# Performance work log

Hardware: AMD Instinct MI355X
Metric: run time of the kernel (lower is better)

Reference implementation:

```python
import jax, jax.numpy as jnp
import numpy as np

T, C, H, N = 1024, 2048, 32, 64
D_LORA, D_G = 64, 128

def _ln(x, w, b, eps=1e-5):
    m = x.mean(-1, keepdims=True)
    v = ((x - m) ** 2).mean(-1, keepdims=True)
    return (x - m) * jax.lax.rsqrt(v + eps) * w + b

def setup_inputs():
    key = jax.random.key(0)
    ks = iter(jax.random.split(key, 48))
    rn = lambda shape, s=1.0: jax.random.normal(next(ks), shape, dtype=jnp.float32) * s
    return {
        "x": rn((T, C)),
        "x_prev_att": rn((C,)),
        "vk_state": rn((H, N, N), 0.1),
        "x_prev_ffn": rn((C,)),
        "v_first": rn((T, C)),
        "ln1_w": jnp.ones((C,), jnp.float32), "ln1_b": jnp.zeros((C,), jnp.float32),
        "x_r": rn((C,), 0.1), "x_w": rn((C,), 0.1), "x_k": rn((C,), 0.1),
        "x_v": rn((C,), 0.1), "x_a": rn((C,), 0.1), "x_g": rn((C,), 0.1),
        "w0": rn((C,), 0.1), "w1": rn((C, D_LORA), 0.02), "w2": rn((D_LORA, C), 0.02),
        "a0": rn((C,), 0.1), "a1": rn((C, D_LORA), 0.02), "a2": rn((D_LORA, C), 0.02),
        "v0": rn((C,), 0.1), "v1": rn((C, D_LORA), 0.02), "v2": rn((D_LORA, C), 0.02),
        "g1": rn((C, D_G), 0.02), "g2": rn((D_G, C), 0.02),
        "k_k": rn((C,), 0.1), "k_a": rn((C,), 0.1), "r_k": rn((C,), 0.1),
        "R_": rn((C, C), 0.02), "K_": rn((C, C), 0.02),
        "V_": rn((C, C), 0.02), "O_": rn((C, C), 0.02),
        "lnx_w": jnp.ones((C,), jnp.float32), "lnx_b": jnp.zeros((C,), jnp.float32),
        "ln2_w": jnp.ones((C,), jnp.float32), "ln2_b": jnp.zeros((C,), jnp.float32),
        "ffn_x_k": rn((C,), 0.1),
        "ffn_K": rn((C, 4 * C), 0.02), "ffn_V": rn((4 * C, C), 0.02),
    }

def reference(x, x_prev_att, vk_state, x_prev_ffn, v_first, ln1_w, ln1_b,
              x_r, x_w, x_k, x_v, x_a, x_g, w0, w1, w2, a0, a1, a2,
              v0, v1, v2, g1, g2, k_k, k_a, r_k, R_, K_, V_, O_,
              lnx_w, lnx_b, ln2_w, ln2_b, ffn_x_k, ffn_K, ffn_V):
    # ---- TMix: RWKV-7 time mixing (layer_id = 1, so v_first blend is active) ----
    xln = _ln(x, ln1_w, ln1_b)                                  # [T, C]
    dx = jnp.concatenate([x_prev_att[None, :], xln[:-1]], axis=0) - xln  # token shift
    xr, xw, xk, xv, xa, xg = (xln + dx * m for m in (x_r, x_w, x_k, x_v, x_a, x_g))
    r = xr @ R_
    w = jnp.tanh(xw @ w1) @ w2
    k = xk @ K_
    v = xv @ V_
    a = jax.nn.sigmoid(a0 + (xa @ a1) @ a2)
    g = jax.nn.sigmoid(xg @ g1) @ g2
    kk = (k * k_k).reshape(T, H, N)
    kk = kk / jnp.maximum(jnp.linalg.norm(kk, axis=-1, keepdims=True), 1e-12)  # L2 normalize per head
    k = k * (1.0 + (a - 1.0) * k_a)
    v = v + (v_first - v) * jax.nn.sigmoid(v0 + (xv @ v1) @ v2)  # layer_id != 0 path
    w = jnp.exp(-0.606531 * jax.nn.sigmoid(w0 + w))               # per-channel decay in (0,1)
    rh, kh, vh = r.reshape(T, H, N), k.reshape(T, H, N), v.reshape(T, H, N)
    ah, wh = a.reshape(T, H, N), w.reshape(T, H, N)

    def step(state, inp):
        # state: [H, N, N]; generalized delta rule: state*w + state@(-kk)(kk*a)^T + v k^T
        w_t, kk_t, a_t, k_t, v_t, r_t = inp
        ab = jnp.einsum('hi,hj->hij', -kk_t, kk_t * a_t)
        vk = jnp.einsum('hi,hj->hij', v_t, k_t)
        state = state * w_t[:, None, :] + jnp.einsum('hij,hjk->hik', state, ab) + vk
        return state, jnp.einsum('hij,hj->hi', state, r_t)

    vk_state, outs = jax.lax.scan(step, vk_state, (wh, kk, ah, kh, vh, rh))  # outs: [T, H, N]
    # group norm over H groups, eps = 0.00064, affine per-channel
    m = outs.mean(-1, keepdims=True)
    var = ((outs - m) ** 2).mean(-1, keepdims=True)
    gn = ((outs - m) * jax.lax.rsqrt(var + 0.00064)).reshape(T, C) * lnx_w + lnx_b
    bonus = ((r * k * r_k).reshape(T, H, N).sum(-1, keepdims=True) * vh).reshape(T, C)
    x = x + ((gn + bonus) * g) @ O_
    # ---- CMix: gated squared-ReLU MLP ----
    xln2 = _ln(x, ln2_w, ln2_b)
    dx2 = jnp.concatenate([x_prev_ffn[None, :], xln2[:-1]], axis=0) - xln2
    kf = jax.nn.relu((xln2 + dx2 * ffn_x_k) @ ffn_K) ** 2
    x = x + kf @ ffn_V
    return x
```

## Files before the change

kernel.cpp:

```cpp
#include <hip/hip_runtime.h>
#include <hip/hip_bf16.h>


#define T_ 1024
#define C_ 2048
#define H_ 32
#define NH 64

typedef __attribute__((ext_vector_type(8))) short short8v;
typedef __attribute__((ext_vector_type(4))) float f32x4;

__device__ __forceinline__ float bf2f(unsigned short u) {
  union { float f; unsigned int i; } c; c.i = ((unsigned int)u) << 16; return c.f;
}
__device__ __forceinline__ unsigned short f2bf(float f) {
  union { float f; unsigned int i; } c; c.f = f;
  unsigned int x = c.i;
  return (unsigned short)((x + 0x7fffu + ((x >> 16) & 1u)) >> 16);
}
__device__ __forceinline__ float sigm(float x) { return 1.f / (1.f + __expf(-x)); }

__device__ __forceinline__ void load8bf(const unsigned short* p, float* o) {
  union { int4 v; unsigned short u[8]; } c;
  c.v = *(const int4*)p;
#pragma unroll
  for (int i = 0; i < 8; ++i) o[i] = bf2f(c.u[i]);
}
__device__ __forceinline__ void store8bf(unsigned short* p, const float* o) {
  union { int4 v; unsigned short u[8]; } c;
#pragma unroll
  for (int i = 0; i < 8; ++i) c.u[i] = f2bf(o[i]);
  *(int4*)p = c.v;
}
__device__ __forceinline__ void load8f(const float* p, float* o) {
  float4 a = ((const float4*)p)[0], b = ((const float4*)p)[1];
  o[0] = a.x; o[1] = a.y; o[2] = a.z; o[3] = a.w;
  o[4] = b.x; o[5] = b.y; o[6] = b.z; o[7] = b.w;
}
__device__ __forceinline__ void load4f(const float* p, float* o) {
  float4 a = *(const float4*)p;
  o[0] = a.x; o[1] = a.y; o[2] = a.z; o[3] = a.w;
}

#define GLD16(g, l)                                                        \
  __builtin_amdgcn_global_load_lds(                                        \
      (const __attribute__((address_space(1))) void*)(g),                  \
      (__attribute__((address_space(3))) void*)(l), 16, 0, 0)

__global__ __launch_bounds__(256) void ln_kernel(const float* __restrict__ x,
                                                 const float* __restrict__ w,
                                                 const float* __restrict__ b,
                                                 unsigned short* __restrict__ out) {
  int t = blockIdx.x, tid = threadIdx.x;
  const float* xr = x + (size_t)t * C_;
  float v[8];
  load8f(xr + tid * 8, v);
  float s = 0.f, q = 0.f;
#pragma unroll
  for (int i = 0; i < 8; ++i) { s += v[i]; q += v[i] * v[i]; }
  for (int m = 1; m < 64; m <<= 1) { s += __shfl_xor(s, m); q += __shfl_xor(q, m); }
  __shared__ float rs[4], rq[4];
  if ((tid & 63) == 0) { rs[tid >> 6] = s; rq[tid >> 6] = q; }
  __syncthreads();
  s = rs[0] + rs[1] + rs[2] + rs[3];
  q = rq[0] + rq[1] + rq[2] + rq[3];
  float mean = s * (1.f / C_);
  float var = q * (1.f / C_) - mean * mean;
  float rstd = rsqrtf(var + 1e-5f);
  int c = tid * 8;
  float o[8];
#pragma unroll
  for (int i = 0; i < 8; ++i) o[i] = (v[i] - mean) * rstd * w[c + i] + b[c + i];
  store8bf(out + (size_t)t * C_ + c, o);
}

__global__ __launch_bounds__(256) void mix6_kernel(
    const unsigned short* __restrict__ xln, const float* __restrict__ xprev,
    const float* __restrict__ mr, const float* __restrict__ mw,
    const float* __restrict__ mk, const float* __restrict__ mv,
    const float* __restrict__ ma, const float* __restrict__ mg,
    unsigned short* xr, unsigned short* xw, unsigned short* xk,
    unsigned short* xv, unsigned short* xa, unsigned short* xg) {
  int t = blockIdx.x, tid = threadIdx.x, c = tid * 8;
  float cur[8], prv[8];
  load8bf(xln + (size_t)t * C_ + c, cur);
  if (t == 0) load8f(xprev + c, prv);
  else load8bf(xln + (size_t)(t - 1) * C_ + c, prv);
  float cf[8], o[8];
  const float* coefs[6] = {mr, mw, mk, mv, ma, mg};
  unsigned short* outs6[6] = {xr, xw, xk, xv, xa, xg};
#pragma unroll
  for (int a = 0; a < 6; ++a) {
    load8f(coefs[a] + c, cf);
#pragma unroll
    for (int i = 0; i < 8; ++i) o[i] = cur[i] + (prv[i] - cur[i]) * cf[i];
    store8bf(outs6[a] + (size_t)t * C_ + c, o);
  }
}

__global__ __launch_bounds__(256) void mix1_kernel(
    const unsigned short* __restrict__ xln, const float* __restrict__ xprev,
    const float* __restrict__ coef, unsigned short* __restrict__ o) {
  int t = blockIdx.x, tid = threadIdx.x, c = tid * 8;
  float cur[8], prv[8], cf[8], o8[8];
  load8bf(xln + (size_t)t * C_ + c, cur);
  if (t == 0) load8f(xprev + c, prv);
  else load8bf(xln + (size_t)(t - 1) * C_ + c, prv);
  load8f(coef + c, cf);
#pragma unroll
  for (int i = 0; i < 8; ++i) o8[i] = cur[i] + (prv[i] - cur[i]) * cf[i];
  store8bf(o + (size_t)t * C_ + c, o8);
}

__global__ __launch_bounds__(256) void transpose_kernel(
    const float* in0, const float* in1, const float* in2,
    unsigned short* o0, unsigned short* o1, unsigned short* o2,
    int R, int Cc) {
  const float* in = blockIdx.z == 0 ? in0 : (blockIdx.z == 1 ? in1 : in2);
  unsigned short* out = blockIdx.z == 0 ? o0 : (blockIdx.z == 1 ? o1 : o2);
  __shared__ __align__(16) unsigned short tile[64][80];
  int c0 = blockIdx.x * 64, r0 = blockIdx.y * 64;
  int rr = threadIdx.x >> 4, cq = threadIdx.x & 15;
#pragma unroll
  for (int i = 0; i < 4; ++i) {
    int r = rr + i * 16;
    float4 v = *(const float4*)(in + (size_t)(r0 + r) * Cc + c0 + cq * 4);
    tile[cq * 4 + 0][r] = f2bf(v.x);
    tile[cq * 4 + 1][r] = f2bf(v.y);
    tile[cq * 4 + 2][r] = f2bf(v.z);
    tile[cq * 4 + 3][r] = f2bf(v.w);
  }
  __syncthreads();
  int cr = threadIdx.x >> 2, rg = threadIdx.x & 3;
  int4 w0 = *(const int4*)&tile[cr][rg * 16];
  int4 w1 = *(const int4*)&tile[cr][rg * 16 + 8];
  unsigned short* op = out + (size_t)(c0 + cr) * R + r0 + rg * 16;
  *(int4*)op = w0;
  *(int4*)(op + 8) = w1;
}

template <int EPI>
__global__ __launch_bounds__(256) void gemm2_kernel(
    const unsigned short* A0, const unsigned short* A1, const unsigned short* A2,
    const unsigned short* B0, const unsigned short* B1, const unsigned short* B2,
    void* C0, void* C1, void* C2, const float* __restrict__ addsrc,
    int M, int K, int N) {
  int z = blockIdx.z;
  const unsigned short* A = z == 0 ? A0 : (z == 1 ? A1 : A2);
  const unsigned short* Bt = z == 0 ? B0 : (z == 1 ? B1 : B2);
  void* Cout = z == 0 ? C0 : (z == 1 ? C1 : C2);
  __shared__ __align__(16) unsigned short As[128 * 32];
  __shared__ __align__(16) unsigned short Bs[128 * 32];
  const int tid = threadIdx.x, lane = tid & 63, wid = tid >> 6;
  const int bm = blockIdx.y * 128, bn = blockIdx.x * 128;
  const int wr = wid >> 1, wc = wid & 1;
  const int mrow = lane & 15, krow = lane >> 4;
  f32x4 acc[4][4] = {};
  for (int kt = 0; kt < K; kt += 32) {
#pragma unroll
    for (int q = 0; q < 2; ++q) {
      int s = q * 2048 + tid * 8;
      int m = s >> 5, k = s & 31;
      GLD16(A + (size_t)(bm + m) * K + kt + k, &As[s]);
      GLD16(Bt + (size_t)(bn + m) * K + kt + k, &Bs[s]);
    }
    __syncthreads();
    short8v af[4], bfrag[4];
#pragma unroll
    for (int i = 0; i < 4; ++i)
      af[i] = *(const short8v*)&As[(wr * 64 + i * 16 + mrow) * 32 + krow * 8];
#pragma unroll
    for (int j = 0; j < 4; ++j)
      bfrag[j] = *(const short8v*)&Bs[(wc * 64 + j * 16 + mrow) * 32 + krow * 8];
#pragma unroll
    for (int i = 0; i < 4; ++i)
#pragma unroll
      for (int j = 0; j < 4; ++j)
        acc[i][j] = __builtin_amdgcn_mfma_f32_16x16x32_bf16(af[i], bfrag[j], acc[i][j], 0, 0, 0);
    __syncthreads();
  }
#pragma unroll
  for (int i = 0; i < 4; ++i)
#pragma unroll
    for (int j = 0; j < 4; ++j)
#pragma unroll
      for (int e = 0; e < 4; ++e) {
        int grow = bm + wr * 64 + i * 16 + (lane >> 4) * 4 + e;
        int gcol = bn + wc * 64 + j * 16 + (lane & 15);
        size_t off = (size_t)grow * N + gcol;
        float v = acc[i][j][e];
        if constexpr (EPI == 0) ((float*)Cout)[off] = v;
        else if constexpr (EPI == 1) ((float*)Cout)[off] = addsrc[off] + v;
        else { float r = v > 0.f ? v : 0.f; ((unsigned short*)Cout)[off] = f2bf(r * r); }
      }
}

__global__ __launch_bounds__(256) void gemm2ks_kernel(
    const unsigned short* __restrict__ A, const unsigned short* __restrict__ Bt,
    float* __restrict__ P, int M, int KH, int Ktot, int N) {
  int kz = blockIdx.z;
  const size_t kbase = (size_t)kz * KH;
  __shared__ __align__(16) unsigned short As[128 * 32];
  __shared__ __align__(16) unsigned short Bs[128 * 32];
  const int tid = threadIdx.x, lane = tid & 63, wid = tid >> 6;
  const int bm = blockIdx.y * 128, bn = blockIdx.x * 128;
  const int wr = wid >> 1, wc = wid & 1;
  const int mrow = lane & 15, krow = lane >> 4;
  f32x4 acc[4][4] = {};
  for (int kt = 0; kt < KH; kt += 32) {
#pragma unroll
    for (int q = 0; q < 2; ++q) {
      int s = q * 2048 + tid * 8;
      int m = s >> 5, k = s & 31;
      GLD16(A + (size_t)(bm + m) * Ktot + kbase + kt + k, &As[s]);
      GLD16(Bt + (size_t)(bn + m) * Ktot + kbase + kt + k, &Bs[s]);
    }
    __syncthreads();
    short8v af[4], bfrag[4];
#pragma unroll
    for (int i = 0; i < 4; ++i)
      af[i] = *(const short8v*)&As[(wr * 64 + i * 16 + mrow) * 32 + krow * 8];
#pragma unroll
    for (int j = 0; j < 4; ++j)
      bfrag[j] = *(const short8v*)&Bs[(wc * 64 + j * 16 + mrow) * 32 + krow * 8];
#pragma unroll
    for (int i = 0; i < 4; ++i)
#pragma unroll
      for (int j = 0; j < 4; ++j)
        acc[i][j] = __builtin_amdgcn_mfma_f32_16x16x32_bf16(af[i], bfrag[j], acc[i][j], 0, 0, 0);
    __syncthreads();
  }
  float* Pz = P + (size_t)kz * M * N;
#pragma unroll
  for (int i = 0; i < 4; ++i)
#pragma unroll
    for (int j = 0; j < 4; ++j)
#pragma unroll
      for (int e = 0; e < 4; ++e) {
        int grow = bm + wr * 64 + i * 16 + (lane >> 4) * 4 + e;
        int gcol = bn + wc * 64 + j * 16 + (lane & 15);
        Pz[(size_t)grow * N + gcol] = acc[i][j][e];
      }
}

__global__ __launch_bounds__(256) void gemm2ks3_kernel(
    const unsigned short* A0, const unsigned short* A1, const unsigned short* A2,
    const unsigned short* B0, const unsigned short* B1, const unsigned short* B2,
    float* __restrict__ P, int M, int KH, int Ktot, int N) {
  int z = blockIdx.z;
  int batch = z % 3, kz = z / 3;
  const unsigned short* A = batch == 0 ? A0 : (batch == 1 ? A1 : A2);
  const unsigned short* Bt = batch == 0 ? B0 : (batch == 1 ? B1 : B2);
  const size_t kbase = (size_t)kz * KH;
  __shared__ __align__(16) unsigned short As[128 * 32];
  __shared__ __align__(16) unsigned short Bs[128 * 32];
  const int tid = threadIdx.x, lane = tid & 63, wid = tid >> 6;
  const int bm = blockIdx.y * 128, bn = blockIdx.x * 128;
  const int wr = wid >> 1, wc = wid & 1;
  const int mrow = lane & 15, krow = lane >> 4;
  f32x4 acc[4][4] = {};
  for (int kt = 0; kt < KH; kt += 32) {
#pragma unroll
    for (int q = 0; q < 2; ++q) {
      int s = q * 2048 + tid * 8;
      int m = s >> 5, k = s & 31;
      GLD16(A + (size_t)(bm + m) * Ktot + kbase + kt + k, &As[s]);
      GLD16(Bt + (size_t)(bn + m) * Ktot + kbase + kt + k, &Bs[s]);
    }
    __syncthreads();
    short8v af[4], bfrag[4];
#pragma unroll
    for (int i = 0; i < 4; ++i)
      af[i] = *(const short8v*)&As[(wr * 64 + i * 16 + mrow) * 32 + krow * 8];
#pragma unroll
    for (int j = 0; j < 4; ++j)
      bfrag[j] = *(const short8v*)&Bs[(wc * 64 + j * 16 + mrow) * 32 + krow * 8];
#pragma unroll
    for (int i = 0; i < 4; ++i)
#pragma unroll
      for (int j = 0; j < 4; ++j)
        acc[i][j] = __builtin_amdgcn_mfma_f32_16x16x32_bf16(af[i], bfrag[j], acc[i][j], 0, 0, 0);
    __syncthreads();
  }
  float* Pz = P + (size_t)z * M * N;
#pragma unroll
  for (int i = 0; i < 4; ++i)
#pragma unroll
    for (int j = 0; j < 4; ++j)
#pragma unroll
      for (int e = 0; e < 4; ++e) {
        int grow = bm + wr * 64 + i * 16 + (lane >> 4) * 4 + e;
        int gcol = bn + wc * 64 + j * 16 + (lane & 15);
        Pz[(size_t)grow * N + gcol] = acc[i][j][e];
      }
}

__global__ __launch_bounds__(256) void addsk3_kernel(float* __restrict__ q) {
  size_t i = ((size_t)blockIdx.x * 256 + threadIdx.x) * 4;
  float4 a = *(const float4*)(q + i);
  float4 b = *(const float4*)(q + i + 3ull * T_ * C_);
  float4 r;
  r.x = a.x + b.x; r.y = a.y + b.y; r.z = a.z + b.z; r.w = a.w + b.w;
  *(float4*)(q + i) = r;
}

__global__ __launch_bounds__(256) void add5_kernel(
    const float* __restrict__ a, const float* __restrict__ p,
    float* __restrict__ o) {
  size_t i = ((size_t)blockIdx.x * 256 + threadIdx.x) * 4;
  const size_t TC = (size_t)T_ * C_;
  float4 va = *(const float4*)(a + i);
  float4 v0 = *(const float4*)(p + i);
  float4 v1 = *(const float4*)(p + i + TC);
  float4 v2 = *(const float4*)(p + i + 2 * TC);
  float4 v3 = *(const float4*)(p + i + 3 * TC);
  float4 r;
  r.x = va.x + v0.x + v1.x + v2.x + v3.x;
  r.y = va.y + v0.y + v1.y + v2.y + v3.y;
  r.z = va.z + v0.z + v1.z + v2.z + v3.z;
  r.w = va.w + v0.w + v1.w + v2.w + v3.w;
  *(float4*)(o + i) = r;
}

__global__ __launch_bounds__(256) void gemm_ks3_kernel(
    const unsigned short* A0, const unsigned short* A1, const unsigned short* A2,
    const unsigned short* B0, const unsigned short* B1, const unsigned short* B2,
    float* P0, float* P1, float* P2, int K, int N) {
  int mz = blockIdx.z >> 3, kz = blockIdx.z & 7;
  const unsigned short* A = mz == 0 ? A0 : (mz == 1 ? A1 : A2);
  const unsigned short* Bt = mz == 0 ? B0 : (mz == 1 ? B1 : B2);
  float* partial = mz == 0 ? P0 : (mz == 1 ? P1 : P2);
  __shared__ __align__(16) unsigned short As[128 * 32];
  __shared__ __align__(16) unsigned short Bs[64 * 32];
  const int tid = threadIdx.x, lane = tid & 63, wid = tid >> 6;
  const int bn = blockIdx.x * 64, bm = blockIdx.y * 128;
  const int wr = wid >> 1, wc = wid & 1;
  const int mrow = lane & 15, krow = lane >> 4;
  f32x4 acc[4][2] = {};
  for (int kt = kz * 256; kt < kz * 256 + 256; kt += 32) {
#pragma unroll
    for (int q = 0; q < 2; ++q) {
      int s = q * 2048 + tid * 8;
      int m = s >> 5, k = s & 31;
      GLD16(A + (size_t)(bm + m) * K + kt + k, &As[s]);
    }
    {
      int s = tid * 8;
      int n = s >> 5, k = s & 31;
      GLD16(Bt + (size_t)(bn + n) * K + kt + k, &Bs[s]);
    }
    __syncthreads();
    short8v af[4], bfrag[2];
#pragma unroll
    for (int i = 0; i < 4; ++i)
      af[i] = *(const short8v*)&As[(wr * 64 + i * 16 + mrow) * 32 + krow * 8];
#pragma unroll
    for (int j = 0; j < 2; ++j)
      bfrag[j] = *(const short8v*)&Bs[(wc * 32 + j * 16 + mrow) * 32 + krow * 8];
#pragma unroll
    for (int i = 0; i < 4; ++i)
#pragma unroll
      for (int j = 0; j < 2; ++j)
        acc[i][j] = __builtin_amdgcn_mfma_f32_16x16x32_bf16(af[i], bfrag[j], acc[i][j], 0, 0, 0);
    __syncthreads();
  }
#pragma unroll
  for (int i = 0; i < 4; ++i)
#pragma unroll
    for (int j = 0; j < 2; ++j)
#pragma unroll
      for (int e = 0; e < 4; ++e) {
        int row = bm + wr * 64 + i * 16 + (lane >> 4) * 4 + e;
        int col = bn + wc * 32 + j * 16 + (lane & 15);
        partial[((size_t)kz * 1024 + row) * N + col] = acc[i][j][e];
      }
}

__global__ __launch_bounds__(256) void gemm_ks_kernel(
    const unsigned short* __restrict__ A, const unsigned short* __restrict__ Bt,
    float* __restrict__ partial, int K, int N) {
  __shared__ __align__(16) unsigned short As[128 * 32];
  __shared__ __align__(16) unsigned short Bs[64 * 32];
  const int tid = threadIdx.x, lane = tid & 63, wid = tid >> 6;
  const int bn = blockIdx.x * 64, bm = blockIdx.y * 128, kz = blockIdx.z;
  const int wr = wid >> 1, wc = wid & 1;
  const int mrow = lane & 15, krow = lane >> 4;
  f32x4 acc[4][2] = {};
  for (int kt = kz * 256; kt < kz * 256 + 256; kt += 32) {
#pragma unroll
    for (int q = 0; q < 2; ++q) {
      int s = q * 2048 + tid * 8;
      int m = s >> 5, k = s & 31;
      GLD16(A + (size_t)(bm + m) * K + kt + k, &As[s]);
    }
    {
      int s = tid * 8;
      int n = s >> 5, k = s & 31;
      GLD16(Bt + (size_t)(bn + n) * K + kt + k, &Bs[s]);
    }
    __syncthreads();
    short8v af[4], bfrag[2];
#pragma unroll
    for (int i = 0; i < 4; ++i)
      af[i] = *(const short8v*)&As[(wr * 64 + i * 16 + mrow) * 32 + krow * 8];
#pragma unroll
    for (int j = 0; j < 2; ++j)
      bfrag[j] = *(const short8v*)&Bs[(wc * 32 + j * 16 + mrow) * 32 + krow * 8];
#pragma unroll
    for (int i = 0; i < 4; ++i)
#pragma unroll
      for (int j = 0; j < 2; ++j)
        acc[i][j] = __builtin_amdgcn_mfma_f32_16x16x32_bf16(af[i], bfrag[j], acc[i][j], 0, 0, 0);
    __syncthreads();
  }
#pragma unroll
  for (int i = 0; i < 4; ++i)
#pragma unroll
    for (int j = 0; j < 2; ++j)
#pragma unroll
      for (int e = 0; e < 4; ++e) {
        int row = bm + wr * 64 + i * 16 + (lane >> 4) * 4 + e;
        int col = bn + wc * 32 + j * 16 + (lane & 15);
        partial[((size_t)kz * 1024 + row) * N + col] = acc[i][j][e];
      }
}

__global__ __launch_bounds__(128) void lora_combine_kernel(
    const float* __restrict__ pw, const float* __restrict__ pa,
    const float* __restrict__ pv, const float* __restrict__ pg,
    unsigned short* __restrict__ hw, unsigned short* __restrict__ ha,
    unsigned short* __restrict__ hv, unsigned short* __restrict__ hg) {
  int t = blockIdx.x, which = blockIdx.y, tid = threadIdx.x;
  int Nl = (which == 3) ? 128 : 64;
  if (tid >= Nl) return;
  const float* p = which == 0 ? pw : which == 1 ? pa : which == 2 ? pv : pg;
  float s = 0.f;
#pragma unroll
  for (int kz = 0; kz < 8; ++kz) s += p[((size_t)kz * 1024 + t) * Nl + tid];
  float r = which == 0 ? tanhf(s) : (which == 3 ? sigm(s) : s);
  unsigned short* o = which == 0 ? hw : which == 1 ? ha : which == 2 ? hv : hg;
  o[t * Nl + tid] = f2bf(r);
}

__global__ __launch_bounds__(256) void post_kernel(
    const float* __restrict__ k_, const float* __restrict__ vraw,
    const float* __restrict__ r_, const float* __restrict__ wpre,
    const float* __restrict__ apre, const float* __restrict__ vpre,
    const float* __restrict__ vfirst, const float* __restrict__ w0,
    const float* __restrict__ a0, const float* __restrict__ v0_,
    const float* __restrict__ k_k, const float* __restrict__ k_a,
    float* __restrict__ scanin) {
  int t = blockIdx.x, tid = threadIdx.x;
  int c = tid * 8, h = tid >> 3, j = c & 63;
  size_t o = (size_t)t * C_ + c;
  float kv[8], vv[8], rv[8], wv[8], av[8], vp[8], vf[8];
  load8f(k_ + o, kv); load8f(vraw + o, vv); load8f(r_ + o, rv);
  load8f(wpre + o, wv); load8f(apre + o, av); load8f(vpre + o, vp);
  load8f(vfirst + o, vf);
  float ckk[8], cka[8], cw0[8], ca0[8], cv0[8];
  load8f(k_k + c, ckk); load8f(k_a + c, cka); load8f(w0 + c, cw0);
  load8f(a0 + c, ca0); load8f(v0_ + c, cv0);
  float kk[8]; float ss = 0.f;
#pragma unroll
  for (int i = 0; i < 8; ++i) { kk[i] = kv[i] * ckk[i]; ss += kk[i] * kk[i]; }
  ss += __shfl_xor(ss, 1); ss += __shfl_xor(ss, 2); ss += __shfl_xor(ss, 4);
  float rdn = 1.f / fmaxf(sqrtf(ss), 1e-12f);
  float sw[8], skn[8], scc[8], sk2[8], sv[8];
#pragma unroll
  for (int i = 0; i < 8; ++i) {
    float kkn = kk[i] * rdn;
    float a = sigm(ca0[i] + av[i]);
    skn[i] = kkn;
    scc[i] = -kkn * a;
    sk2[i] = kv[i] * (1.f + (a - 1.f) * cka[i]);
    float sg = sigm(cv0[i] + vp[i]);
    sv[i] = vv[i] + (vf[i] - vv[i]) * sg;
    sw[i] = __expf(-0.606531f * sigm(cw0[i] + wv[i]));
  }
  float* bp = scanin + ((size_t)h * T_ + t) * 384 + j;
  ((float4*)(bp + 0))[0]   = make_float4(sw[0], sw[1], sw[2], sw[3]);
  ((float4*)(bp + 4))[0]   = make_float4(sw[4], sw[5], sw[6], sw[7]);
  ((float4*)(bp + 64))[0]  = make_float4(skn[0], skn[1], skn[2], skn[3]);
  ((float4*)(bp + 68))[0]  = make_float4(skn[4], skn[5], skn[6], skn[7]);
  ((float4*)(bp + 128))[0] = make_float4(scc[0], scc[1], scc[2], scc[3]);
  ((float4*)(bp + 132))[0] = make_float4(scc[4], scc[5], scc[6], scc[7]);
  ((float4*)(bp + 192))[0] = make_float4(sk2[0], sk2[1], sk2[2], sk2[3]);
  ((float4*)(bp + 196))[0] = make_float4(sk2[4], sk2[5], sk2[6], sk2[7]);
  ((float4*)(bp + 256))[0] = make_float4(sv[0], sv[1], sv[2], sv[3]);
  ((float4*)(bp + 260))[0] = make_float4(sv[4], sv[5], sv[6], sv[7]);
  ((float4*)(bp + 320))[0] = make_float4(rv[0], rv[1], rv[2], rv[3]);
  ((float4*)(bp + 324))[0] = make_float4(rv[4], rv[5], rv[6], rv[7]);
}

struct SR { float wv[4], nv[4], cv[4], kv[4], rv[4], vvv; };

template <int CTRL>
__device__ __forceinline__ float dppadd(float x) {
  int y = __builtin_amdgcn_update_dpp(0, __float_as_int(x), CTRL, 0xF, 0xF, true);
  return x + __int_as_float(y);
}
__device__ __forceinline__ float red16(float x) {
  x = dppadd<0xB1>(x);
  x = dppadd<0x4E>(x);
  x = dppadd<0x140>(x);
  x = dppadd<0x141>(x);
  return x;
}

__device__ __forceinline__ void loadstep(const float* S, SR& R, int p4, int row) {
  load4f(S + p4, R.wv);
  load4f(S + 64 + p4, R.nv);
  load4f(S + 128 + p4, R.cv);
  load4f(S + 192 + p4, R.kv);
  load4f(S + 320 + p4, R.rv);
  R.vvv = S[256 + row];
}

__device__ __forceinline__ void stepcomp(const SR& R, float* st, int part,
                                         float* __restrict__ ob, size_t oidx) {
  float p0 = fmaf(st[0], R.nv[0], 0.f);
  float p1 = fmaf(st[1], R.nv[1], 0.f);
  p0 = fmaf(st[2], R.nv[2], p0);
  p1 = fmaf(st[3], R.nv[3], p1);
  float sa = red16(p0 + p1);
  float s0 = 0.f, s1 = 0.f;
#pragma unroll
  for (int i = 0; i < 4; ++i) {
    float t = fmaf(st[i], R.wv[i], fmaf(sa, R.cv[i], R.vvv * R.kv[i]));
    st[i] = t;
    if (i & 1) s1 = fmaf(t, R.rv[i], s1);
    else s0 = fmaf(t, R.rv[i], s0);
  }
  float so = red16(s0 + s1);
  if (part == 0) ob[oidx] = so;
}

__global__ __launch_bounds__(64) void scan5_kernel(
    const float* __restrict__ scanin, const float* __restrict__ vk0,
    float* __restrict__ outs) {
  int bid = blockIdx.x;
  int h = (bid & 7) + 8 * ((bid >> 3) & 3);
  int rg = bid >> 5;
  int tid = threadIdx.x;
  int part = tid & 15, row = rg * 4 + (tid >> 4);
  int p4 = part * 4;
  float st[4];
  load4f(vk0 + ((size_t)h * NH + row) * NH + p4, st);
  const float* src = scanin + (size_t)h * T_ * 384;
  float* ob = outs + h * NH + row;
  SR A, B, C, D;
  loadstep(src + 0 * 384, A, p4, row);
  loadstep(src + 1 * 384, B, p4, row);
  loadstep(src + 2 * 384, C, p4, row);
  int s = 0;
  for (; s < T_ - 4; s += 4) {
    const float* sp = src + (size_t)s * 384;
    loadstep(sp + 3 * 384, D, p4, row);
    stepcomp(A, st, part, ob, (size_t)(s + 0) * C_);
    loadstep(sp + 4 * 384, A, p4, row);
    stepcomp(B, st, part, ob, (size_t)(s + 1) * C_);
    loadstep(sp + 5 * 384, B, p4, row);
    stepcomp(C, st, part, ob, (size_t)(s + 2) * C_);
    loadstep(sp + 6 * 384, C, p4, row);
    stepcomp(D, st, part, ob, (size_t)(s + 3) * C_);
  }
  loadstep(src + (size_t)(T_ - 1) * 384, D, p4, row);
  stepcomp(A, st, part, ob, (size_t)(s + 0) * C_);
  stepcomp(B, st, part, ob, (size_t)(s + 1) * C_);
  stepcomp(C, st, part, ob, (size_t)(s + 2) * C_);
  stepcomp(D, st, part, ob, (size_t)(s + 3) * C_);
}

__global__ __launch_bounds__(256) void gnb_kernel(
    const float* __restrict__ outs, const float* __restrict__ scanin,
    const float* __restrict__ g, const float* __restrict__ rk,
    const float* __restrict__ gw, const float* __restrict__ gb,
    unsigned short* __restrict__ attin) {
  int t = blockIdx.x, tid = threadIdx.x;
  int c = tid * 8, h = tid >> 3, j = c & 63;
  float o[8], gv[8], rkv[8];
  load8f(outs + (size_t)t * C_ + c, o);
  load8f(g + (size_t)t * C_ + c, gv);
  load8f(rk + c, rkv);
  size_t sbase = ((size_t)h * T_ + t) * 384 + j;
  float rv[8], k2[8], vv[8];
  load8f(scanin + sbase + 320, rv);
  load8f(scanin + sbase + 192, k2);
  load8f(scanin + sbase + 256, vv);
  float s = 0.f, q = 0.f, bs = 0.f;
#pragma unroll
  for (int i = 0; i < 8; ++i) {
    s += o[i]; q += o[i] * o[i];
    bs += rv[i] * k2[i] * rkv[i];
  }
  s += __shfl_xor(s, 1); s += __shfl_xor(s, 2); s += __shfl_xor(s, 4);
  q += __shfl_xor(q, 1); q += __shfl_xor(q, 2); q += __shfl_xor(q, 4);
  bs += __shfl_xor(bs, 1); bs += __shfl_xor(bs, 2); bs += __shfl_xor(bs, 4);
  float mean = s * (1.f / NH);
  float var = q * (1.f / NH) - mean * mean;
  float rstd = rsqrtf(var + 0.00064f);
  float res[8];
#pragma unroll
  for (int i = 0; i < 8; ++i) {
    float gn = (o[i] - mean) * rstd * gw[c + i] + gb[c + i];
    res[i] = (gn + bs * vv[i]) * gv[i];
  }
  store8bf(attin + (size_t)t * C_ + c, res);
}

extern "C" void kernel_launch(void* const* d_in, const int* in_sizes, int n_in,
                              void* d_out, int out_size, void* d_ws, size_t ws_size,
                              hipStream_t stream) {
  const float* x       = (const float*)d_in[0];
  const float* xprev_a = (const float*)d_in[1];
  const float* vk0     = (const float*)d_in[2];
  const float* xprev_f = (const float*)d_in[3];
  const float* vfirst  = (const float*)d_in[4];
  const float* ln1w = (const float*)d_in[5];
  const float* ln1b = (const float*)d_in[6];
  const float* m_r = (const float*)d_in[7];
  const float* m_w = (const float*)d_in[8];
  const float* m_k = (const float*)d_in[9];
  const float* m_v = (const float*)d_in[10];
  const float* m_a = (const float*)d_in[11];
  const float* m_g = (const float*)d_in[12];
  const float* w0 = (const float*)d_in[13];
  const float* w1 = (const float*)d_in[14];
  const float* w2 = (const float*)d_in[15];
  const float* a0 = (const float*)d_in[16];
  const float* a1 = (const float*)d_in[17];
  const float* a2 = (const float*)d_in[18];
  const float* v0 = (const float*)d_in[19];
  const float* v1 = (const float*)d_in[20];
  const float* v2 = (const float*)d_in[21];
  const float* g1 = (const float*)d_in[22];
  const float* g2 = (const float*)d_in[23];
  const float* k_k = (const float*)d_in[24];
  const float* k_a = (const float*)d_in[25];
  const float* r_k = (const float*)d_in[26];
  const float* R_ = (const float*)d_in[27];
  const float* K_ = (const float*)d_in[28];
  const float* V_ = (const float*)d_in[29];
  const float* O_ = (const float*)d_in[30];
  const float* lnxw = (const float*)d_in[31];
  const float* lnxb = (const float*)d_in[32];
  const float* ln2w = (const float*)d_in[33];
  const float* ln2b = (const float*)d_in[34];
  const float* fxk = (const float*)d_in[35];
  const float* fK = (const float*)d_in[36];
  const float* fV = (const float*)d_in[37];
  float* out = (float*)d_out;

  char* ws = (char*)d_ws;
  const size_t MB = 1ull << 20;
  unsigned short* xln   = (unsigned short*)(ws + 0 * MB);
  unsigned short* attin = (unsigned short*)(ws + 0 * MB);
  unsigned short* xr    = (unsigned short*)(ws + 4 * MB);
  unsigned short* xln2  = (unsigned short*)(ws + 4 * MB);
  unsigned short* xw    = (unsigned short*)(ws + 8 * MB);
  unsigned short* xkf   = (unsigned short*)(ws + 8 * MB);
  unsigned short* xk    = (unsigned short*)(ws + 12 * MB);
  unsigned short* xv    = (unsigned short*)(ws + 16 * MB);
  unsigned short* xa    = (unsigned short*)(ws + 20 * MB);
  unsigned short* xg    = (unsigned short*)(ws + 24 * MB);
  float* qRKV  = (float*)(ws + 28 * MB);
  float* r_buf = (float*)(ws + 28 * MB);
  float* k_buf = (float*)(ws + 36 * MB);
  float* v_buf = (float*)(ws + 44 * MB);
  unsigned short* fVt = (unsigned short*)(ws + 28 * MB);
  float* wpre  = (float*)(ws + 52 * MB);
  float* outsb = (float*)(ws + 52 * MB);
  float* apre  = (float*)(ws + 60 * MB);
  float* x_att = (float*)(ws + 60 * MB);
  float* vpre  = (float*)(ws + 68 * MB);
  float* g_buf = (float*)(ws + 76 * MB);
  float* scanin = (float*)(ws + 84 * MB);
  unsigned short* Rt  = (unsigned short*)(ws + 84 * MB);
  unsigned short* Kt  = (unsigned short*)(ws + 92 * MB);
  unsigned short* Vt  = (unsigned short*)(ws + 100 * MB);
  unsigned short* Ot  = (unsigned short*)(ws + 84 * MB);
  float* qO = (float*)(ws + 92 * MB);
  unsigned short* hffn = (unsigned short*)(ws + 84 * MB);
  unsigned short* fKt  = (unsigned short*)(ws + 100 * MB);
  float* pF = (float*)(ws + 100 * MB);
  unsigned short* w1t = (unsigned short*)(ws + 0);
  unsigned short* a1t = (unsigned short*)(ws + 262144);
  unsigned short* v1t = (unsigned short*)(ws + 524288);
  unsigned short* g1t = (unsigned short*)(ws + 786432);
  unsigned short* hwb = (unsigned short*)(ws + 1310720);
  unsigned short* hab = (unsigned short*)(ws + 1441792);
  unsigned short* hvb = (unsigned short*)(ws + 1572864);
  unsigned short* hgb = (unsigned short*)(ws + 1703936);
  float* pw = (float*)(ws + 2 * MB);
  float* pa = (float*)(ws + 4 * MB);
  float* pv = (float*)(ws + 6 * MB);
  float* pg = (float*)(ws + 8 * MB);
  unsigned short* w2t = (unsigned short*)(ws + 12 * MB);
  unsigned short* a2t = (unsigned short*)(ws + 12 * MB + 262144);
  unsigned short* v2t = (unsigned short*)(ws + 12 * MB + 524288);
  unsigned short* g2t = (unsigned short*)(ws + 12 * MB + 786432);

  ln_kernel<<<T_, 256, 0, stream>>>(x, ln1w, ln1b, xln);
  mix6_kernel<<<T_, 256, 0, stream>>>(xln, xprev_a, m_r, m_w, m_k, m_v, m_a, m_g,
                                      xr, xw, xk, xv, xa, xg);
  transpose_kernel<<<dim3(32, 32, 3), 256, 0, stream>>>(R_, K_, V_, Rt, Kt, Vt, C_, C_);
  gemm2ks3_kernel<<<dim3(16, 8, 6), 256, 0, stream>>>(xr, xk, xv, Rt, Kt, Vt,
                                                      qRKV, T_, 1024, C_, C_);
  addsk3_kernel<<<6144, 256, 0, stream>>>(qRKV);
  transpose_kernel<<<dim3(1, 32, 3), 256, 0, stream>>>(w1, a1, v1, w1t, a1t, v1t, C_, 64);
  transpose_kernel<<<dim3(2, 32, 1), 256, 0, stream>>>(g1, g1, g1, g1t, g1t, g1t, C_, 128);
  gemm_ks3_kernel<<<dim3(1, 8, 24), 256, 0, stream>>>(xw, xa, xv, w1t, a1t, v1t,
                                                      pw, pa, pv, C_, 64);
  gemm_ks_kernel<<<dim3(2, 8, 8), 256, 0, stream>>>(xg, g1t, pg, C_, 128);
  lora_combine_kernel<<<dim3(T_, 4), 128, 0, stream>>>(pw, pa, pv, pg, hwb, hab, hvb, hgb);
  transpose_kernel<<<dim3(32, 1, 3), 256, 0, stream>>>(w2, a2, v2, w2t, a2t, v2t, 64, C_);
  transpose_kernel<<<dim3(32, 2, 1), 256, 0, stream>>>(g2, g2, g2, g2t, g2t, g2t, 128, C_);
  gemm2_kernel<0><<<dim3(16, 8, 3), 256, 0, stream>>>(hwb, hab, hvb, w2t, a2t, v2t,
                                                      wpre, apre, vpre, nullptr, T_, 64, C_);
  gemm2_kernel<0><<<dim3(16, 8, 1), 256, 0, stream>>>(hgb, hgb, hgb, g2t, g2t, g2t,
                                                      g_buf, g_buf, g_buf, nullptr, T_, 128, C_);
  post_kernel<<<T_, 256, 0, stream>>>(k_buf, v_buf, r_buf, wpre, apre, vpre, vfirst,
                                      w0, a0, v0, k_k, k_a, scanin);
  scan5_kernel<<<512, 64, 0, stream>>>(scanin, vk0, outsb);
  gnb_kernel<<<T_, 256, 0, stream>>>(outsb, scanin, g_buf, r_k, lnxw, lnxb, attin);
  transpose_kernel<<<dim3(32, 32, 1), 256, 0, stream>>>(O_, O_, O_, Ot, Ot, Ot, C_, C_);
  transpose_kernel<<<dim3(32, 128, 1), 256, 0, stream>>>(fV, fV, fV, fVt, fVt, fVt, 4 * C_, C_);
  gemm2ks_kernel<<<dim3(16, 8, 4), 256, 0, stream>>>(attin, Ot, qO, T_, 512, C_, C_);
  add5_kernel<<<2048, 256, 0, stream>>>(x, qO, x_att);
  ln_kernel<<<T_, 256, 0, stream>>>(x_att, ln2w, ln2b, xln2);
  mix1_kernel<<<T_, 256, 0, stream>>>(xln2, xprev_f, fxk, xkf);
  transpose_kernel<<<dim3(128, 32, 1), 256, 0, stream>>>(fK, fK, fK, fKt, fKt, fKt, C_, 4 * C_);
  gemm2_kernel<2><<<dim3(64, 8, 1), 256, 0, stream>>>(xkf, xkf, xkf, fKt, fKt, fKt,
                                                      hffn, hffn, hffn, nullptr, T_, C_, 4 * C_);
  gemm2ks_kernel<<<dim3(16, 8, 4), 256, 0, stream>>>(hffn, fVt, pF, T_, 2048, 4 * C_, C_);
  add5_kernel<<<2048, 256, 0, stream>>>(x_att, pF, out);
}
```

Before: 514.0 us.

## Double-buffer LDS tiles in all MFMA GEMM kernels to overlap loads with compute

Each bf16 MFMA GEMM variant (batched, split-K and 64-wide split-K) now keeps two LDS buffers for the A and B tiles. The loads for the next K-slice are issued at the top of each iteration, before the MFMA work on the current slice, which drops one barrier per iteration. The aim is to hide global-to-LDS latency behind matrix-core work. In exchange, LDS per block doubles, which may lower how many blocks fit on a CU at once.

```diff
diff --git a/kernel.cpp b/kernel.cpp
--- a/kernel.cpp
+++ b/kernel.cpp
@@ -149,35 +149,41 @@
   const unsigned short* A = z == 0 ? A0 : (z == 1 ? A1 : A2);
   const unsigned short* Bt = z == 0 ? B0 : (z == 1 ? B1 : B2);
   void* Cout = z == 0 ? C0 : (z == 1 ? C1 : C2);
-  __shared__ __align__(16) unsigned short As[128 * 32];
-  __shared__ __align__(16) unsigned short Bs[128 * 32];
+  __shared__ __align__(16) unsigned short As[2][128 * 32];
+  __shared__ __align__(16) unsigned short Bs[2][128 * 32];
   const int tid = threadIdx.x, lane = tid & 63, wid = tid >> 6;
   const int bm = blockIdx.y * 128, bn = blockIdx.x * 128;
   const int wr = wid >> 1, wc = wid & 1;
   const int mrow = lane & 15, krow = lane >> 4;
-  f32x4 acc[4][4] = {};
-  for (int kt = 0; kt < K; kt += 32) {
+  auto stage = [&](int buf, int kt) {
 #pragma unroll
     for (int q = 0; q < 2; ++q) {
       int s = q * 2048 + tid * 8;
       int m = s >> 5, k = s & 31;
-      GLD16(A + (size_t)(bm + m) * K + kt + k, &As[s]);
-      GLD16(Bt + (size_t)(bn + m) * K + kt + k, &Bs[s]);
+      GLD16(A + (size_t)(bm + m) * K + kt + k, &As[buf][s]);
+      GLD16(Bt + (size_t)(bn + m) * K + kt + k, &Bs[buf][s]);
     }
-    __syncthreads();
+  };
+  f32x4 acc[4][4] = {};
+  stage(0, 0);
+  __syncthreads();
+  int buf = 0;
+  for (int kt = 0; kt < K; kt += 32) {
+    if (kt + 32 < K) stage(buf ^ 1, kt + 32);
     short8v af[4], bfrag[4];
 #pragma unroll
     for (int i = 0; i < 4; ++i)
-      af[i] = *(const short8v*)&As[(wr * 64 + i * 16 + mrow) * 32 + krow * 8];
+      af[i] = *(const short8v*)&As[buf][(wr * 64 + i * 16 + mrow) * 32 + krow * 8];
 #pragma unroll
     for (int j = 0; j < 4; ++j)
-      bfrag[j] = *(const short8v*)&Bs[(wc * 64 + j * 16 + mrow) * 32 + krow * 8];
+      bfrag[j] = *(const short8v*)&Bs[buf][(wc * 64 + j * 16 + mrow) * 32 + krow * 8];
 #pragma unroll
     for (int i = 0; i < 4; ++i)
 #pragma unroll
       for (int j = 0; j < 4; ++j)
         acc[i][j] = __builtin_amdgcn_mfma_f32_16x16x32_bf16(af[i], bfrag[j], acc[i][j], 0, 0, 0);
     __syncthreads();
+    buf ^= 1;
   }
 #pragma unroll
   for (int i = 0; i < 4; ++i)
@@ -200,35 +206,41 @@
     float* __restrict__ P, int M, int KH, int Ktot, int N) {
   int kz = blockIdx.z;
   const size_t kbase = (size_t)kz * KH;
-  __shared__ __align__(16) unsigned short As[128 * 32];
-  __shared__ __align__(16) unsigned short Bs[128 * 32];
+  __shared__ __align__(16) unsigned short As[2][128 * 32];
+  __shared__ __align__(16) unsigned short Bs[2][128 * 32];
   const int tid = threadIdx.x, lane = tid & 63, wid = tid >> 6;
   const int bm = blockIdx.y * 128, bn = blockIdx.x * 128;
   const int wr = wid >> 1, wc = wid & 1;
   const int mrow = lane & 15, krow = lane >> 4;
-  f32x4 acc[4][4] = {};
-  for (int kt = 0; kt < KH; kt += 32) {
+  auto stage = [&](int buf, int kt) {
 #pragma unroll
     for (int q = 0; q < 2; ++q) {
       int s = q * 2048 + tid * 8;
       int m = s >> 5, k = s & 31;
-      GLD16(A + (size_t)(bm + m) * Ktot + kbase + kt + k, &As[s]);
-      GLD16(Bt + (size_t)(bn + m) * Ktot + kbase + kt + k, &Bs[s]);
+      GLD16(A + (size_t)(bm + m) * Ktot + kbase + kt + k, &As[buf][s]);
+      GLD16(Bt + (size_t)(bn + m) * Ktot + kbase + kt + k, &Bs[buf][s]);
     }
-    __syncthreads();
+  };
+  f32x4 acc[4][4] = {};
+  stage(0, 0);
+  __syncthreads();
+  int buf = 0;
+  for (int kt = 0; kt < KH; kt += 32) {
+    if (kt + 32 < KH) stage(buf ^ 1, kt + 32);
     short8v af[4], bfrag[4];
 #pragma unroll
     for (int i = 0; i < 4; ++i)
-      af[i] = *(const short8v*)&As[(wr * 64 + i * 16 + mrow) * 32 + krow * 8];
+      af[i] = *(const short8v*)&As[buf][(wr * 64 + i * 16 + mrow) * 32 + krow * 8];
 #pragma unroll
     for (int j = 0; j < 4; ++j)
-      bfrag[j] = *(const short8v*)&Bs[(wc * 64 + j * 16 + mrow) * 32 + krow * 8];
+      bfrag[j] = *(const short8v*)&Bs[buf][(wc * 64 + j * 16 + mrow) * 32 + krow * 8];
 #pragma unroll
     for (int i = 0; i < 4; ++i)
 #pragma unroll
       for (int j = 0; j < 4; ++j)
         acc[i][j] = __builtin_amdgcn_mfma_f32_16x16x32_bf16(af[i], bfrag[j], acc[i][j], 0, 0, 0);
     __syncthreads();
+    buf ^= 1;
   }
   float* Pz = P + (size_t)kz * M * N;
 #pragma unroll
@@ -252,35 +264,41 @@
   const unsigned short* A = batch == 0 ? A0 : (batch == 1 ? A1 : A2);
   const unsigned short* Bt = batch == 0 ? B0 : (batch == 1 ? B1 : B2);
   const size_t kbase = (size_t)kz * KH;
-  __shared__ __align__(16) unsigned short As[128 * 32];
-  __shared__ __align__(16) unsigned short Bs[128 * 32];
+  __shared__ __align__(16) unsigned short As[2][128 * 32];
+  __shared__ __align__(16) unsigned short Bs[2][128 * 32];
   const int tid = threadIdx.x, lane = tid & 63, wid = tid >> 6;
   const int bm = blockIdx.y * 128, bn = blockIdx.x * 128;
   const int wr = wid >> 1, wc = wid & 1;
   const int mrow = lane & 15, krow = lane >> 4;
-  f32x4 acc[4][4] = {};
-  for (int kt = 0; kt < KH; kt += 32) {
+  auto stage = [&](int buf, int kt) {
 #pragma unroll
     for (int q = 0; q < 2; ++q) {
       int s = q * 2048 + tid * 8;
       int m = s >> 5, k = s & 31;
-      GLD16(A + (size_t)(bm + m) * Ktot + kbase + kt + k, &As[s]);
-      GLD16(Bt + (size_t)(bn + m) * Ktot + kbase + kt + k, &Bs[s]);
+      GLD16(A + (size_t)(bm + m) * Ktot + kbase + kt + k, &As[buf][s]);
+      GLD16(Bt + (size_t)(bn + m) * Ktot + kbase + kt + k, &Bs[buf][s]);
     }
-    __syncthreads();
+  };
+  f32x4 acc[4][4] = {};
+  stage(0, 0);
+  __syncthreads();
+  int buf = 0;
+  for (int kt = 0; kt < KH; kt += 32) {
+    if (kt + 32 < KH) stage(buf ^ 1, kt + 32);
     short8v af[4], bfrag[4];
 #pragma unroll
     for (int i = 0; i < 4; ++i)
-      af[i] = *(const short8v*)&As[(wr * 64 + i * 16 + mrow) * 32 + krow * 8];
+      af[i] = *(const short8v*)&As[buf][(wr * 64 + i * 16 + mrow) * 32 + krow * 8];
 #pragma unroll
     for (int j = 0; j < 4; ++j)
-      bfrag[j] = *(const short8v*)&Bs[(wc * 64 + j * 16 + mrow) * 32 + krow * 8];
+      bfrag[j] = *(const short8v*)&Bs[buf][(wc * 64 + j * 16 + mrow) * 32 + krow * 8];
 #pragma unroll
     for (int i = 0; i < 4; ++i)
 #pragma unroll
       for (int j = 0; j < 4; ++j)
         acc[i][j] = __builtin_amdgcn_mfma_f32_16x16x32_bf16(af[i], bfrag[j], acc[i][j], 0, 0, 0);
     __syncthreads();
+    buf ^= 1;
   }
   float* Pz = P + (size_t)z * M * N;
 #pragma unroll
@@ -330,39 +348,46 @@
   const unsigned short* A = mz == 0 ? A0 : (mz == 1 ? A1 : A2);
   const unsigned short* Bt = mz == 0 ? B0 : (mz == 1 ? B1 : B2);
   float* partial = mz == 0 ? P0 : (mz == 1 ? P1 : P2);
-  __shared__ __align__(16) unsigned short As[128 * 32];
-  __shared__ __align__(16) unsigned short Bs[64 * 32];
+  __shared__ __align__(16) unsigned short As[2][128 * 32];
+  __shared__ __align__(16) unsigned short Bs[2][64 * 32];
   const int tid = threadIdx.x, lane = tid & 63, wid = tid >> 6;
   const int bn = blockIdx.x * 64, bm = blockIdx.y * 128;
   const int wr = wid >> 1, wc = wid & 1;
   const int mrow = lane & 15, krow = lane >> 4;
-  f32x4 acc[4][2] = {};
-  for (int kt = kz * 256; kt < kz * 256 + 256; kt += 32) {
+  auto stage = [&](int buf, int kt) {
 #pragma unroll
     for (int q = 0; q < 2; ++q) {
       int s = q * 2048 + tid * 8;
       int m = s >> 5, k = s & 31;
-      GLD16(A + (size_t)(bm + m) * K + kt + k, &As[s]);
+      GLD16(A + (size_t)(bm + m) * K + kt + k, &As[buf][s]);
     }
     {
       int s = tid * 8;
       int n = s >> 5, k = s & 31;
-      GLD16(Bt + (size_t)(bn + n) * K + kt + k, &Bs[s]);
+      GLD16(Bt + (size_t)(bn + n) * K + kt + k, &Bs[buf][s]);
     }
-    __syncthreads();
+  };
+  f32x4 acc[4][2] = {};
+  int k0 = kz * 256;
+  stage(0, k0);
+  __syncthreads();
+  int buf = 0;
+  for (int kt = k0; kt < k0 + 256; kt += 32) {
+    if (kt + 32 < k0 + 256) stage(buf ^ 1, kt + 32);
     short8v af[4], bfrag[2];
 #pragma unroll
     for (int i = 0; i < 4; ++i)
-      af[i] = *(const short8v*)&As[(wr * 64 + i * 16 + mrow) * 32 + krow * 8];
+      af[i] = *(const short8v*)&As[buf][(wr * 64 + i * 16 + mrow) * 32 + krow * 8];
 #pragma unroll
     for (int j = 0; j < 2; ++j)
-      bfrag[j] = *(const short8v*)&Bs[(wc * 32 + j * 16 + mrow) * 32 + krow * 8];
+      bfrag[j] = *(const short8v*)&Bs[buf][(wc * 32 + j * 16 + mrow) * 32 + krow * 8];
 #pragma unroll
     for (int i = 0; i < 4; ++i)
 #pragma unroll
       for (int j = 0; j < 2; ++j)
         acc[i][j] = __builtin_amdgcn_mfma_f32_16x16x32_bf16(af[i], bfrag[j], acc[i][j], 0, 0, 0);
     __syncthreads();
+    buf ^= 1;
   }
 #pragma unroll
   for (int i = 0; i < 4; ++i)
@@ -379,39 +404,46 @@
 __global__ __launch_bounds__(256) void gemm_ks_kernel(
     const unsigned short* __restrict__ A, const unsigned short* __restrict__ Bt,
     float* __restrict__ partial, int K, int N) {
-  __shared__ __align__(16) unsigned short As[128 * 32];
-  __shared__ __align__(16) unsigned short Bs[64 * 32];
+  __shared__ __align__(16) unsigned short As[2][128 * 32];
+  __shared__ __align__(16) unsigned short Bs[2][64 * 32];
   const int tid = threadIdx.x, lane = tid & 63, wid = tid >> 6;
   const int bn = blockIdx.x * 64, bm = blockIdx.y * 128, kz = blockIdx.z;
   const int wr = wid >> 1, wc = wid & 1;
   const int mrow = lane & 15, krow = lane >> 4;
-  f32x4 acc[4][2] = {};
-  for (int kt = kz * 256; kt < kz * 256 + 256; kt += 32) {
+  auto stage = [&](int buf, int kt) {
 #pragma unroll
     for (int q = 0; q < 2; ++q) {
       int s = q * 2048 + tid * 8;
       int m = s >> 5, k = s & 31;
-      GLD16(A + (size_t)(bm + m) * K + kt + k, &As[s]);
+      GLD16(A + (size_t)(bm + m) * K + kt + k, &As[buf][s]);
     }
     {
       int s = tid * 8;
       int n = s >> 5, k = s & 31;
-      GLD16(Bt + (size_t)(bn + n) * K + kt + k, &Bs[s]);
+      GLD16(Bt + (size_t)(bn + n) * K + kt + k, &Bs[buf][s]);
     }
-    __syncthreads();
+  };
+  f32x4 acc[4][2] = {};
+  int k0 = kz * 256;
+  stage(0, k0);
+  __syncthreads();
+  int buf = 0;
+  for (int kt = k0; kt < k0 + 256; kt += 32) {
+    if (kt + 32 < k0 + 256) stage(buf ^ 1, kt + 32);
     short8v af[4], bfrag[2];
 #pragma unroll
     for (int i = 0; i < 4; ++i)
-      af[i] = *(const short8v*)&As[(wr * 64 + i * 16 + mrow) * 32 + krow * 8];
+      af[i] = *(const short8v*)&As[buf][(wr * 64 + i * 16 + mrow) * 32 + krow * 8];
 #pragma unroll
     for (int j = 0; j < 2; ++j)
-      bfrag[j] = *(const short8v*)&Bs[(wc * 32 + j * 16 + mrow) * 32 + krow * 8];
+      bfrag[j] = *(const short8v*)&Bs[buf][(wc * 32 + j * 16 + mrow) * 32 + krow * 8];
 #pragma unroll
     for (int i = 0; i < 4; ++i)
 #pragma unroll
       for (int j = 0; j < 2; ++j)
         acc[i][j] = __builtin_amdgcn_mfma_f32_16x16x32_bf16(af[i], bfrag[j], acc[i][j], 0, 0, 0);
     __syncthreads();
+    buf ^= 1;
   }
 #pragma unroll
   for (int i = 0; i < 4; ++i)
```

Measured after the change: 495.3 us. 1.04x faster.
